# Kernel tuning notes

Hardware: AMD Instinct MI355X
Metric: run time of the kernel (lower is better)

The kernel has to match this reference:

```python
import jax, jax.numpy as jnp
import numpy as np

EPS = 1e-8  # torch F.cosine_similarity eps
TEMP = 2.0  # hardcoded in module regardless of init arg


def _normalize(x):
    # row-normalize with torch-style eps clamp on the norm
    norm = jnp.sqrt(jnp.sum(x * x, axis=-1, keepdims=True))
    return x / jnp.maximum(norm, EPS)


def setup_inputs() -> dict:
    key = jax.random.key(0)
    k1, k2, k3 = jax.random.split(key, 3)
    n, m, d = 8192, 8192, 256
    return {
        "pos_key": jax.random.normal(k1, (n, d), dtype=jnp.float32),
        "pos_value": jax.random.normal(k2, (n, d), dtype=jnp.float32),
        "neg_value": jax.random.normal(k3, (m, d), dtype=jnp.float32),
    }


def reference(pos_key, pos_value, neg_value):
    pk = _normalize(pos_key)    # [n, d]
    pv = _normalize(pos_value)  # [n, d]
    nv = _normalize(neg_value)  # [m, d]

    pos_sim = jnp.sum(pk * pv, axis=-1)          # [n]
    neg_sim = jnp.einsum("nd,md->nm", pk, nv)    # [n, m] cosine sims

    pos_loss = -jnp.mean(pos_sim / TEMP)
    # log-sum-exp over m (stable), matching log(sum(exp(.)))
    neg_loss = jnp.mean(jax.scipy.special.logsumexp(neg_sim / TEMP, axis=-1))
    return pos_loss + neg_loss
```

## Files before the change

kernel.cpp:

```cpp
#include <hip/hip_runtime.h>

typedef __attribute__((ext_vector_type(4))) float f32x4;
typedef __attribute__((ext_vector_type(4))) int   i32x4;
typedef __attribute__((ext_vector_type(8))) int   i32x8;

#define DIM 256
#define D4  64

#define GLD_LDS16(g, l) __builtin_amdgcn_global_load_lds(                      \
    (const __attribute__((address_space(1))) void*)(g),                        \
    (__attribute__((address_space(3))) void*)(l), 16, 0, 0)

__global__ __launch_bounds__(256) void normalize_kernel(
    const float4* __restrict__ pk, const float4* __restrict__ pv,
    const float4* __restrict__ nv, unsigned int* __restrict__ pkn,
    unsigned int* __restrict__ nvn, float* __restrict__ posPart, int N) {
  int row  = blockIdx.x * 4 + (threadIdx.x >> 6);
  int lane = threadIdx.x & 63;
  if (row < N) {
    float4 x = pk[row * D4 + lane];
    float4 y = pv[row * D4 + lane];
    float skk = x.x*x.x + x.y*x.y + x.z*x.z + x.w*x.w;
    float svv = y.x*y.x + y.y*y.y + y.z*y.z + y.w*y.w;
    float skv = x.x*y.x + x.y*y.y + x.z*y.z + x.w*y.w;
#pragma unroll
    for (int m = 32; m >= 1; m >>= 1) {
      skk += __shfl_xor(skk, m, 64);
      svv += __shfl_xor(svv, m, 64);
      skv += __shfl_xor(skv, m, 64);
    }
    float nk  = fmaxf(sqrtf(skk), 1e-8f);
    float nvv = fmaxf(sqrtf(svv), 1e-8f);
    if (lane == 0) posPart[row] = skv / (nk * nvv);
    float rk = 1.0f / nk;
    int w = __builtin_amdgcn_cvt_pk_fp8_f32(x.x * rk, x.y * rk, 0, false);
    w = __builtin_amdgcn_cvt_pk_fp8_f32(x.z * rk, x.w * rk, w, true);
    pkn[(size_t)row * 64 + lane] = (unsigned int)w;
  } else {
    int r2 = row - N;
    float4 x = nv[r2 * D4 + lane];
    float s = x.x*x.x + x.y*x.y + x.z*x.z + x.w*x.w;
#pragma unroll
    for (int m = 32; m >= 1; m >>= 1) s += __shfl_xor(s, m, 64);
    float rn = 1.0f / fmaxf(sqrtf(s), 1e-8f);
    int w = __builtin_amdgcn_cvt_pk_fp8_f32(x.x * rn, x.y * rn, 0, false);
    w = __builtin_amdgcn_cvt_pk_fp8_f32(x.z * rn, x.w * rn, w, true);
    nvn[(size_t)r2 * 64 + lane] = (unsigned int)w;
  }
}

__global__ __launch_bounds__(512, 2) void gemm_lse_kernel(
    const unsigned char* __restrict__ gA, const unsigned char* __restrict__ gB,
    float* __restrict__ partial, int N) {
  __shared__ unsigned char As[65536];
  __shared__ unsigned char Bs[65536];

  const int tid  = threadIdx.x;
  const int lane = tid & 63;
  const int wv   = tid >> 6;
  const int wm   = wv >> 2;
  const int wn   = wv & 3;
  const int l15  = lane & 15, q = lane >> 4;
  const int row0 = blockIdx.y * 256;
  const int col0 = blockIdx.x * 256;
  const float kLog2eHalf = 0.72134752044448170f;
  const int kUnitScale = 0x7F7F7F7F;

  f32x4 acc[8][4];
#pragma unroll
  for (int mi = 0; mi < 8; mi++)
#pragma unroll
    for (int ni = 0; ni < 4; ni++) acc[mi][ni] = (f32x4){0.f, 0.f, 0.f, 0.f};

#pragma unroll
  for (int kb = 0; kb < 2; kb++)
#pragma unroll
    for (int i = 0; i < 4; i++) {
      int c  = i * 512 + tid;
      int r  = c >> 3;
      int sc = ((c & 7) ^ (r & 7)) << 4;
      GLD_LDS16(gA + (size_t)(row0 + r) * 256 + kb * 128 + sc,
                As + kb * 32768 + c * 16);
      GLD_LDS16(gB + (size_t)(col0 + r) * 256 + kb * 128 + sc,
                Bs + kb * 32768 + c * 16);
    }

#pragma unroll
  for (int kb = 0; kb < 2; kb++) {
    if (kb == 0) asm volatile("s_waitcnt vmcnt(8)\n\ts_barrier" ::: "memory");
    else         asm volatile("s_waitcnt vmcnt(0)\n\ts_barrier" ::: "memory");

    const int kbo = kb * 32768;
    i32x8 bf[4];
#pragma unroll
    for (int ni = 0; ni < 4; ni++) {
      int r  = wn * 64 + ni * 16 + l15;
      int c0 = (q * 2)     ^ (r & 7);
      int c1 = (q * 2 + 1) ^ (r & 7);
      i32x4 lo = *(const i32x4*)(Bs + kbo + r * 128 + c0 * 16);
      i32x4 hi = *(const i32x4*)(Bs + kbo + r * 128 + c1 * 16);
      bf[ni] = (i32x8){lo.x, lo.y, lo.z, lo.w, hi.x, hi.y, hi.z, hi.w};
    }
#pragma unroll
    for (int mi = 0; mi < 8; mi++) {
      int r  = wm * 128 + mi * 16 + l15;
      int c0 = (q * 2)     ^ (r & 7);
      int c1 = (q * 2 + 1) ^ (r & 7);
      i32x4 lo = *(const i32x4*)(As + kbo + r * 128 + c0 * 16);
      i32x4 hi = *(const i32x4*)(As + kbo + r * 128 + c1 * 16);
      i32x8 af = (i32x8){lo.x, lo.y, lo.z, lo.w, hi.x, hi.y, hi.z, hi.w};
      __builtin_amdgcn_s_setprio(1);
#pragma unroll
      for (int ni = 0; ni < 4; ni++)
        acc[mi][ni] = __builtin_amdgcn_mfma_scale_f32_16x16x128_f8f6f4(
            bf[ni], af, acc[mi][ni],
            0, 0, 0, kUnitScale, 0, kUnitScale);
      __builtin_amdgcn_s_setprio(0);
    }
  }

  float s[8];
#pragma unroll
  for (int mi = 0; mi < 8; mi++) {
    float v = 0.f;
#pragma unroll
    for (int ni = 0; ni < 4; ni++)
#pragma unroll
      for (int rr = 0; rr < 4; rr++)
        v += __builtin_amdgcn_exp2f(acc[mi][ni][rr] * kLog2eHalf);
    v += __shfl_xor(v, 16, 64);
    v += __shfl_xor(v, 32, 64);
    s[mi] = v;
  }
  float o0 = q == 0 ? s[0] : q == 1 ? s[1] : q == 2 ? s[2] : s[3];
  float o1 = q == 0 ? s[4] : q == 1 ? s[5] : q == 2 ? s[6] : s[7];
  size_t slab = (size_t)(blockIdx.x * 4 + wn);
  int r0 = row0 + wm * 128 + q * 16 + l15;
  partial[slab * N + r0]      = o0;
  partial[slab * N + r0 + 64] = o1;
}

__global__ __launch_bounds__(256) void finalize_kernel(
    const float* __restrict__ partial, const float* __restrict__ posPart,
    float* __restrict__ out, int N, int slabsPerGroup, float invN) {
  __shared__ float red[4][64];
  int t  = threadIdx.x;
  int rl = t & 63, g = t >> 6;
  int row = blockIdx.x * 64 + rl;
  const float* p = partial + (size_t)(g * slabsPerGroup) * N + row;
  float s = 0.f;
#pragma unroll 8
  for (int j = 0; j < slabsPerGroup; j++) s += p[(size_t)j * N];
  red[g][rl] = s;
  __syncthreads();
  if (t < 64) {
    float tot = red[0][rl] + red[1][rl] + red[2][rl] + red[3][rl];
    float v = __builtin_amdgcn_logf(tot) * 0.69314718055994531f
              - 0.5f * posPart[row];
#pragma unroll
    for (int m = 32; m >= 1; m >>= 1) v += __shfl_xor(v, m, 64);
    if (rl == 0) atomicAdd(out, v * invN);
  }
}

extern "C" void kernel_launch(void* const* d_in, const int* in_sizes, int n_in,
                              void* d_out, int out_size, void* d_ws, size_t ws_size,
                              hipStream_t stream) {
  const float* pk = (const float*)d_in[0];
  const float* pv = (const float*)d_in[1];
  const float* nv = (const float*)d_in[2];
  int N = in_sizes[0] / DIM;
  int M = in_sizes[2] / DIM;
  float* out = (float*)d_out;

  unsigned char* pkn = (unsigned char*)d_ws;
  unsigned char* nvn = pkn + (size_t)N * DIM;
  float* partial = (float*)(nvn + (size_t)M * DIM);
  float* posPart = partial + (size_t)(M / 64) * N;

  hipMemsetAsync(out, 0, sizeof(float), stream);

  normalize_kernel<<<(N + M) / 4, 256, 0, stream>>>(
      (const float4*)pk, (const float4*)pv, (const float4*)nv,
      (unsigned int*)pkn, (unsigned int*)nvn, posPart, N);

  gemm_lse_kernel<<<dim3(M / 256, N / 256), 512, 0, stream>>>(
      pkn, nvn, partial, N);

  finalize_kernel<<<N / 64, 256, 0, stream>>>(
      partial, posPart, out, N, (M / 64) / 4, 1.0f / (float)N);
}
```

Measured before the change: 103.8 us.

## Make GEMM blocks persistent over column panels with double-buffered B tiles

Each block now keeps its 256-row A panel resident in LDS and loops over eight 128-column B tiles, double-buffering B loads so they overlap the MFMA and exp epilogue of the previous tile. The warp layout changes to 4x2 with smaller per-warp accumulators (4x4), which lowers register pressure. A is reloaded far less often. The grid shrinks fourfold to 256 blocks, which may leave CUs underfilled, and there is an extra barrier per tile. Partial slab indexing is kept compatible with finalize (16 slabs per 1024 columns).

```diff
diff --git a/kernel.cpp b/kernel.cpp
--- a/kernel.cpp
+++ b/kernel.cpp
@@ -53,24 +53,35 @@
     const unsigned char* __restrict__ gA, const unsigned char* __restrict__ gB,
     float* __restrict__ partial, int N) {
   __shared__ unsigned char As[65536];
-  __shared__ unsigned char Bs[65536];
+  __shared__ unsigned char Bs[2][32768];
 
   const int tid  = threadIdx.x;
   const int lane = tid & 63;
   const int wv   = tid >> 6;
-  const int wm   = wv >> 2;
-  const int wn   = wv & 3;
+  const int wm   = wv >> 1;
+  const int wn   = wv & 1;
   const int l15  = lane & 15, q = lane >> 4;
-  const int row0 = blockIdx.y * 256;
-  const int col0 = blockIdx.x * 256;
+  const int cg    = blockIdx.x;
+  const int panel = blockIdx.y;
+  const int row0  = panel * 256;
+  const int colBase = cg * 1024;
   const float kLog2eHalf = 0.72134752044448170f;
   const int kUnitScale = 0x7F7F7F7F;
 
-  f32x4 acc[8][4];
-#pragma unroll
-  for (int mi = 0; mi < 8; mi++)
-#pragma unroll
-    for (int ni = 0; ni < 4; ni++) acc[mi][ni] = (f32x4){0.f, 0.f, 0.f, 0.f};
+  auto stageB = [&](int t) {
+    const unsigned char* src = gB + (size_t)(colBase + t * 128) * 256;
+    unsigned char* dst = &Bs[t & 1][0];
+#pragma unroll
+    for (int kb = 0; kb < 2; kb++)
+#pragma unroll
+      for (int i = 0; i < 2; i++) {
+        int c  = i * 512 + tid;
+        int r  = c >> 3;
+        int sc = ((c & 7) ^ (r & 7)) << 4;
+        GLD_LDS16(src + (size_t)r * 256 + kb * 128 + sc,
+                  dst + kb * 16384 + c * 16);
+      }
+  };
 
 #pragma unroll
   for (int kb = 0; kb < 2; kb++)
@@ -81,63 +92,73 @@
       int sc = ((c & 7) ^ (r & 7)) << 4;
       GLD_LDS16(gA + (size_t)(row0 + r) * 256 + kb * 128 + sc,
                 As + kb * 32768 + c * 16);
-      GLD_LDS16(gB + (size_t)(col0 + r) * 256 + kb * 128 + sc,
-                Bs + kb * 32768 + c * 16);
-    }
-
-#pragma unroll
-  for (int kb = 0; kb < 2; kb++) {
-    if (kb == 0) asm volatile("s_waitcnt vmcnt(8)\n\ts_barrier" ::: "memory");
-    else         asm volatile("s_waitcnt vmcnt(0)\n\ts_barrier" ::: "memory");
-
-    const int kbo = kb * 32768;
-    i32x8 bf[4];
-#pragma unroll
-    for (int ni = 0; ni < 4; ni++) {
-      int r  = wn * 64 + ni * 16 + l15;
-      int c0 = (q * 2)     ^ (r & 7);
-      int c1 = (q * 2 + 1) ^ (r & 7);
-      i32x4 lo = *(const i32x4*)(Bs + kbo + r * 128 + c0 * 16);
-      i32x4 hi = *(const i32x4*)(Bs + kbo + r * 128 + c1 * 16);
-      bf[ni] = (i32x8){lo.x, lo.y, lo.z, lo.w, hi.x, hi.y, hi.z, hi.w};
-    }
-#pragma unroll
-    for (int mi = 0; mi < 8; mi++) {
-      int r  = wm * 128 + mi * 16 + l15;
-      int c0 = (q * 2)     ^ (r & 7);
-      int c1 = (q * 2 + 1) ^ (r & 7);
-      i32x4 lo = *(const i32x4*)(As + kbo + r * 128 + c0 * 16);
-      i32x4 hi = *(const i32x4*)(As + kbo + r * 128 + c1 * 16);
-      i32x8 af = (i32x8){lo.x, lo.y, lo.z, lo.w, hi.x, hi.y, hi.z, hi.w};
-      __builtin_amdgcn_s_setprio(1);
+    }
+  stageB(0);
+  stageB(1);
+  asm volatile("s_waitcnt vmcnt(4)\n\ts_barrier" ::: "memory");
+
+#pragma unroll 2
+  for (int t = 0; t < 8; t++) {
+    if (t) {
+      asm volatile("s_waitcnt vmcnt(1)\n\ts_barrier" ::: "memory");
+      if (t < 7) stageB(t + 1);
+    }
+    const unsigned char* bufB = &Bs[t & 1][0];
+
+    f32x4 acc[4][4];
+#pragma unroll
+    for (int mi = 0; mi < 4; mi++)
+#pragma unroll
+      for (int ni = 0; ni < 4; ni++) acc[mi][ni] = (f32x4){0.f, 0.f, 0.f, 0.f};
+
+#pragma unroll
+    for (int kb = 0; kb < 2; kb++) {
+      i32x8 bf[4];
+#pragma unroll
+      for (int ni = 0; ni < 4; ni++) {
+        int r  = wn * 64 + ni * 16 + l15;
+        int c0 = (q * 2)     ^ (r & 7);
+        int c1 = (q * 2 + 1) ^ (r & 7);
+        i32x4 lo = *(const i32x4*)(bufB + kb * 16384 + r * 128 + c0 * 16);
+        i32x4 hi = *(const i32x4*)(bufB + kb * 16384 + r * 128 + c1 * 16);
+        bf[ni] = (i32x8){lo.x, lo.y, lo.z, lo.w, hi.x, hi.y, hi.z, hi.w};
+      }
+#pragma unroll
+      for (int mi = 0; mi < 4; mi++) {
+        int r  = wm * 64 + mi * 16 + l15;
+        int c0 = (q * 2)     ^ (r & 7);
+        int c1 = (q * 2 + 1) ^ (r & 7);
+        i32x4 lo = *(const i32x4*)(As + kb * 32768 + r * 128 + c0 * 16);
+        i32x4 hi = *(const i32x4*)(As + kb * 32768 + r * 128 + c1 * 16);
+        i32x8 af = (i32x8){lo.x, lo.y, lo.z, lo.w, hi.x, hi.y, hi.z, hi.w};
+        __builtin_amdgcn_s_setprio(1);
+#pragma unroll
+        for (int ni = 0; ni < 4; ni++)
+          acc[mi][ni] = __builtin_amdgcn_mfma_scale_f32_16x16x128_f8f6f4(
+              bf[ni], af, acc[mi][ni],
+              0, 0, 0, kUnitScale, 0, kUnitScale);
+        __builtin_amdgcn_s_setprio(0);
+      }
+    }
+
+    float s0, s1, s2, s3;
+#pragma unroll
+    for (int mi = 0; mi < 4; mi++) {
+      float v = 0.f;
 #pragma unroll
       for (int ni = 0; ni < 4; ni++)
-        acc[mi][ni] = __builtin_amdgcn_mfma_scale_f32_16x16x128_f8f6f4(
-            bf[ni], af, acc[mi][ni],
-            0, 0, 0, kUnitScale, 0, kUnitScale);
-      __builtin_amdgcn_s_setprio(0);
-    }
+#pragma unroll
+        for (int rr = 0; rr < 4; rr++)
+          v += __builtin_amdgcn_exp2f(acc[mi][ni][rr] * kLog2eHalf);
+      v += __shfl_xor(v, 16, 64);
+      v += __shfl_xor(v, 32, 64);
+      if (mi == 0) s0 = v; else if (mi == 1) s1 = v;
+      else if (mi == 2) s2 = v; else s3 = v;
+    }
+    float o = q == 0 ? s0 : q == 1 ? s1 : q == 2 ? s2 : s3;
+    int slab = cg * 16 + t * 2 + wn;
+    partial[(size_t)slab * N + row0 + wm * 64 + q * 16 + l15] = o;
   }
-
-  float s[8];
-#pragma unroll
-  for (int mi = 0; mi < 8; mi++) {
-    float v = 0.f;
-#pragma unroll
-    for (int ni = 0; ni < 4; ni++)
-#pragma unroll
-      for (int rr = 0; rr < 4; rr++)
-        v += __builtin_amdgcn_exp2f(acc[mi][ni][rr] * kLog2eHalf);
-    v += __shfl_xor(v, 16, 64);
-    v += __shfl_xor(v, 32, 64);
-    s[mi] = v;
-  }
-  float o0 = q == 0 ? s[0] : q == 1 ? s[1] : q == 2 ? s[2] : s[3];
-  float o1 = q == 0 ? s[4] : q == 1 ? s[5] : q == 2 ? s[6] : s[7];
-  size_t slab = (size_t)(blockIdx.x * 4 + wn);
-  int r0 = row0 + wm * 128 + q * 16 + l15;
-  partial[slab * N + r0]      = o0;
-  partial[slab * N + r0 + 64] = o1;
 }
 
 __global__ __launch_bounds__(256) void finalize_kernel(
@@ -184,7 +205,7 @@
       (const float4*)pk, (const float4*)pv, (const float4*)nv,
       (unsigned int*)pkn, (unsigned int*)nvn, posPart, N);
 
-  gemm_lse_kernel<<<dim3(M / 256, N / 256), 512, 0, stream>>>(
+  gemm_lse_kernel<<<dim3(M / 1024, N / 256), 512, 0, stream>>>(
       pkn, nvn, partial, N);
 
   finalize_kernel<<<N / 64, 256, 0, stream>>>(
```

Result: faster. 101.0 us (-2.7%).
